# Kernel optimization log

Measured on AMD Instinct MI355X. Metric: run time of the kernel, lower is better.

## Reference

```python
import jax, jax.numpy as jnp
import numpy as np

ALPHA = 0.2  # LeakyReLU negative slope
NEG_INF = -9e15


def setup_inputs() -> dict:
    key = jax.random.key(0)
    k1, k2, k3, k4 = jax.random.split(key, 4)
    B, N, F_IN, F_OUT = 2, 4096, 128, 64
    h = jax.random.normal(k1, (B, N, F_IN), dtype=jnp.float32)
    adj = jax.random.randint(k2, (N, N), 0, 2, dtype=jnp.int32)
    W = jax.random.normal(k3, (F_IN, F_OUT), dtype=jnp.float32) * (1.414 / np.sqrt(F_IN))
    a = jax.random.normal(k4, (2 * F_OUT, 1), dtype=jnp.float32) * 0.1
    return {"h": h, "adj": adj, "W": W, "a": a}


def reference(h, adj, W, a):
    # h: (B, N, F_in), adj: (N, N), W: (F_in, F_out), a: (2*F_out, 1)
    Wh = jnp.einsum("bnf,fo->bno", h, W)  # (B, N, F_out)
    F_out = W.shape[1]
    a1 = a[:F_out, 0]   # attends to source node i
    a2 = a[F_out:, 0]   # attends to target node j
    # e_ij = leakyrelu(a1.Wh_i + a2.Wh_j)  -- rank-1 decomposition of the
    # original cat([Wh_i, Wh_j]) @ a, identical math without O(N^2*2F) tensor.
    s1 = Wh @ a1  # (B, N)
    s2 = Wh @ a2  # (B, N)
    e = s1[:, :, None] + s2[:, None, :]  # (B, N, N)
    e = jnp.where(e >= 0, e, ALPHA * e)  # LeakyReLU
    scores = jnp.where(adj[None, :, :] > 0, e, NEG_INF)
    attention = jax.nn.softmax(scores, axis=-1)
    # dropout=0 (eval/deterministic baseline)
    h_prime = jnp.einsum("bij,bjo->bio", attention, Wh)  # (B, N, F_out)
    return jax.nn.elu(h_prime)  # concat=True branch
```

## Files before the change

kernel.cpp:

```cpp
#include <hip/hip_runtime.h>
#include <hip/hip_bf16.h>
#include <math.h>

#define NB 2
#define NN 4096
#define FIN 128
#define FOUT 64
#define LALPHA 0.2f

#define WS_S1   0
#define WS_S2   (NB*NN)
#define WS_WHT  (2*NB*NN)

typedef __attribute__((ext_vector_type(8))) short short8;
typedef __attribute__((ext_vector_type(4))) float f32x4;

static __device__ inline unsigned int pack2bf(float x, float y) {
    float2 f2; f2.x = x; f2.y = y;
    __hip_bfloat162 pp = __float22bfloat162_rn(f2);
    return *reinterpret_cast<unsigned int*>(&pp);
}

__global__ __launch_bounds__(256) void k1_proj(const float* __restrict__ h,
                                               const float* __restrict__ W,
                                               const float* __restrict__ a,
                                               float* __restrict__ ws) {
    __shared__ float tbuf[4][68];
    int gid  = blockIdx.x * 256 + threadIdx.x;
    int wid  = gid >> 6;
    int lane = threadIdx.x & 63;
    int w    = threadIdx.x >> 6;
    const float* hrow = h + (size_t)wid * FIN;
    float h0 = hrow[lane];
    float h1 = hrow[64 + lane];
    float acc = 0.f;
#pragma unroll
    for (int f = 0; f < 64; ++f) {
        float hf = __shfl(h0, f);
        acc = fmaf(hf, W[f * FOUT + lane], acc);
    }
#pragma unroll
    for (int f = 0; f < 64; ++f) {
        float hf = __shfl(h1, f);
        acc = fmaf(hf, W[(64 + f) * FOUT + lane], acc);
    }
    tbuf[w][lane] = acc;
    float v1 = acc * a[lane];
    float v2 = acc * a[FOUT + lane];
#pragma unroll
    for (int off = 32; off; off >>= 1) {
        v1 += __shfl_xor(v1, off);
        v2 += __shfl_xor(v2, off);
    }
    if (lane == 0) {
        ws[WS_S1 + wid] = v1;
        ws[WS_S2 + wid] = v2;
    }
    __syncthreads();
    if (threadIdx.x < 64) {
        int f = threadIdx.x;
        int wid0 = blockIdx.x * 4;
        int b  = wid0 >> 12;
        int n0 = wid0 & (NN - 1);
        unsigned short* whT = (unsigned short*)(ws + WS_WHT);
        uint2 pk;
        pk.x = pack2bf(tbuf[0][f], tbuf[1][f]);
        pk.y = pack2bf(tbuf[2][f], tbuf[3][f]);
        *(uint2*)&whT[(size_t)(b * FOUT + f) * NN + n0] = pk;
    }
}

__global__ __launch_bounds__(1024, 4) void k3_attn(const int* __restrict__ adj,
                                                   const float* __restrict__ ws,
                                                   float* __restrict__ out) {
    __shared__ float red[16][2048];
    __shared__ float lred[16][32];
    const int tid  = threadIdx.x;
    const int w    = tid >> 6;
    const int lane = tid & 63;
    const int col  = lane & 15;
    const int quad = lane >> 4;
    const int rt   = blockIdx.x;
    const int i0   = rt * 16;
    const int jbase = w * 256;

    const float* __restrict__ s1 = ws + WS_S1;
    const float* __restrict__ s2 = ws + WS_S2;
    const unsigned short* __restrict__ whT = (const unsigned short*)(ws + WS_WHT);

    float s1a[2];
#pragma unroll
    for (int b = 0; b < 2; ++b) s1a[b] = s1[b * NN + i0 + col];

    f32x4 acc[2][4];
    float lsum[2] = {0.f, 0.f};
#pragma unroll
    for (int b = 0; b < 2; ++b)
#pragma unroll
        for (int nt = 0; nt < 4; ++nt) acc[b][nt] = (f32x4)0.f;

#pragma unroll
    for (int ks = 0; ks < 8; ++ks) {
        const int j8 = jbase + ks * 32 + quad * 8;
        int4 ava = *(const int4*)&adj[(size_t)(i0 + col) * NN + j8];
        int4 avb = *(const int4*)&adj[(size_t)(i0 + col) * NN + j8 + 4];
        int am[8] = {ava.x, ava.y, ava.z, ava.w, avb.x, avb.y, avb.z, avb.w};
#pragma unroll
        for (int b = 0; b < 2; ++b) {
            float4 s2lo = *(const float4*)&s2[b * NN + j8];
            float4 s2hi = *(const float4*)&s2[b * NN + j8 + 4];
            float sj[8] = {s2lo.x, s2lo.y, s2lo.z, s2lo.w,
                           s2hi.x, s2hi.y, s2hi.z, s2hi.w};
            float p[8];
#pragma unroll
            for (int jj = 0; jj < 8; ++jj) {
                float e = s1a[b] + sj[jj];
                e = fmaxf(e, LALPHA * e);
                float pe = __expf(e);
                p[jj] = am[jj] > 0 ? pe : 0.f;
                lsum[b] += p[jj];
            }
            unsigned int pk[4];
#pragma unroll
            for (int q = 0; q < 4; ++q) pk[q] = pack2bf(p[2 * q], p[2 * q + 1]);
            short8 afrag = *(short8*)pk;
#pragma unroll
            for (int nt = 0; nt < 4; ++nt) {
                short8 bfrag = *(const short8*)
                    &whT[(size_t)(b * FOUT + nt * 16 + col) * NN + j8];
                acc[b][nt] = __builtin_amdgcn_mfma_f32_16x16x32_bf16(
                    afrag, bfrag, acc[b][nt], 0, 0, 0);
            }
        }
    }

#pragma unroll
    for (int b = 0; b < 2; ++b) {
        float v = lsum[b];
        v += __shfl_xor(v, 16);
        v += __shfl_xor(v, 32);
        if (quad == 0) lred[w][b * 16 + col] = v;
#pragma unroll
        for (int nt = 0; nt < 4; ++nt)
#pragma unroll
            for (int reg = 0; reg < 4; ++reg)
                red[w][(((b * 4 + nt) * 4 + reg) << 6) + lane] = acc[b][nt][reg];
    }
    __syncthreads();

#pragma unroll
    for (int e = 0; e < 2; ++e) {
        int flat = e * 1024 + tid;
        int f    = flat & 63;
        int r16  = (flat >> 6) & 15;
        int b    = flat >> 10;
        int q2   = r16 >> 2, reg = r16 & 3;
        int c2   = f & 15,   nt  = f >> 4;
        int ln   = q2 * 16 + c2;
        int off  = (((b * 4 + nt) * 4 + reg) << 6) + ln;
        float acv = 0.f, l = 0.f;
#pragma unroll
        for (int ww = 0; ww < 16; ++ww) {
            acv += red[ww][off];
            l   += lred[ww][b * 16 + r16];
        }
        float v = acv / l;
        out[(size_t)(((b * NN) + i0 + r16) << 6) + f] = v > 0.f ? v : (__expf(v) - 1.f);
    }
}

extern "C" void kernel_launch(void* const* d_in, const int* in_sizes, int n_in,
                              void* d_out, int out_size, void* d_ws, size_t ws_size,
                              hipStream_t stream) {
    const float* h   = (const float*)d_in[0];
    const int*   adj = (const int*)d_in[1];
    const float* W   = (const float*)d_in[2];
    const float* a   = (const float*)d_in[3];
    float* ws  = (float*)d_ws;
    float* out = (float*)d_out;

    hipLaunchKernelGGL(k1_proj, dim3(NB * NN / 4), dim3(256), 0, stream, h, W, a, ws);
    hipLaunchKernelGGL(k3_attn, dim3(256), dim3(1024), 0, stream, adj, ws, out);
}
```

Baseline: 150.4 us.

## Prepack adjacency into bitmask in projection kernel, read bits in attention

The projection kernel now also reads the int32 adjacency matrix and packs it into a 1-bit-per-edge mask in workspace, using its many small blocks. The attention kernel loads eight 32-bit words per lane instead of streaming int4 adjacency loads inside its inner loop. The aim is to move the large adjacency read out of the low-occupancy attention kernel, where it stalls the MFMA loop, into a kernel that has more parallelism. The trade-off is an extra write and read of the bitmask, plus more work and register pressure in k1. The mask test also changes from adj > 0 to adj != 0.

```diff
diff --git a/kernel.cpp b/kernel.cpp
--- a/kernel.cpp
+++ b/kernel.cpp
@@ -8,9 +8,10 @@
 #define FOUT 64
 #define LALPHA 0.2f
 
-#define WS_S1   0
-#define WS_S2   (NB*NN)
-#define WS_WHT  (2*NB*NN)
+#define WS_S1    0
+#define WS_S2    (NB*NN)
+#define WS_WHT   (2*NB*NN)
+#define WS_ABITS (WS_WHT + NB*FOUT*NN/2)
 
 typedef __attribute__((ext_vector_type(8))) short short8;
 typedef __attribute__((ext_vector_type(4))) float f32x4;
@@ -24,12 +25,21 @@
 __global__ __launch_bounds__(256) void k1_proj(const float* __restrict__ h,
                                                const float* __restrict__ W,
                                                const float* __restrict__ a,
+                                               const int* __restrict__ adj,
                                                float* __restrict__ ws) {
     __shared__ float tbuf[4][68];
     int gid  = blockIdx.x * 256 + threadIdx.x;
     int wid  = gid >> 6;
     int lane = threadIdx.x & 63;
     int w    = threadIdx.x >> 6;
+
+    int prow  = 2 * blockIdx.x + (threadIdx.x >> 7);
+    int pword = threadIdx.x & 127;
+    const int4* psrc = (const int4*)&adj[(size_t)prow * NN + pword * 32];
+    int4 pv[8];
+#pragma unroll
+    for (int k = 0; k < 8; ++k) pv[k] = psrc[k];
+
     const float* hrow = h + (size_t)wid * FIN;
     float h0 = hrow[lane];
     float h1 = hrow[64 + lane];
@@ -56,6 +66,17 @@
         ws[WS_S1 + wid] = v1;
         ws[WS_S2 + wid] = v2;
     }
+
+    unsigned int bits = 0;
+#pragma unroll
+    for (int k = 0; k < 8; ++k) {
+        bits |= (pv[k].x != 0 ? 1u : 0u) << (4 * k);
+        bits |= (pv[k].y != 0 ? 1u : 0u) << (4 * k + 1);
+        bits |= (pv[k].z != 0 ? 1u : 0u) << (4 * k + 2);
+        bits |= (pv[k].w != 0 ? 1u : 0u) << (4 * k + 3);
+    }
+    ((unsigned int*)(ws + WS_ABITS))[(size_t)prow * 128 + pword] = bits;
+
     __syncthreads();
     if (threadIdx.x < 64) {
         int f = threadIdx.x;
@@ -70,8 +91,7 @@
     }
 }
 
-__global__ __launch_bounds__(1024, 4) void k3_attn(const int* __restrict__ adj,
-                                                   const float* __restrict__ ws,
+__global__ __launch_bounds__(1024, 4) void k3_attn(const float* __restrict__ ws,
                                                    float* __restrict__ out) {
     __shared__ float red[16][2048];
     __shared__ float lred[16][32];
@@ -87,6 +107,14 @@
     const float* __restrict__ s1 = ws + WS_S1;
     const float* __restrict__ s2 = ws + WS_S2;
     const unsigned short* __restrict__ whT = (const unsigned short*)(ws + WS_WHT);
+    const unsigned int* __restrict__ abits = (const unsigned int*)(ws + WS_ABITS);
+
+    unsigned int mrow[8];
+    {
+        const int4* mp = (const int4*)&abits[(size_t)(i0 + col) * 128 + w * 8];
+        *(int4*)&mrow[0] = mp[0];
+        *(int4*)&mrow[4] = mp[1];
+    }
 
     float s1a[2];
 #pragma unroll
@@ -102,9 +130,7 @@
 #pragma unroll
     for (int ks = 0; ks < 8; ++ks) {
         const int j8 = jbase + ks * 32 + quad * 8;
-        int4 ava = *(const int4*)&adj[(size_t)(i0 + col) * NN + j8];
-        int4 avb = *(const int4*)&adj[(size_t)(i0 + col) * NN + j8 + 4];
-        int am[8] = {ava.x, ava.y, ava.z, ava.w, avb.x, avb.y, avb.z, avb.w};
+        const unsigned int mb = (mrow[ks] >> (quad * 8)) & 0xffu;
 #pragma unroll
         for (int b = 0; b < 2; ++b) {
             float4 s2lo = *(const float4*)&s2[b * NN + j8];
@@ -117,7 +143,7 @@
                 float e = s1a[b] + sj[jj];
                 e = fmaxf(e, LALPHA * e);
                 float pe = __expf(e);
-                p[jj] = am[jj] > 0 ? pe : 0.f;
+                p[jj] = ((mb >> jj) & 1u) ? pe : 0.f;
                 lsum[b] += p[jj];
             }
             unsigned int pk[4];
@@ -179,6 +205,6 @@
     float* ws  = (float*)d_ws;
     float* out = (float*)d_out;
 
-    hipLaunchKernelGGL(k1_proj, dim3(NB * NN / 4), dim3(256), 0, stream, h, W, a, ws);
-    hipLaunchKernelGGL(k3_attn, dim3(256), dim3(1024), 0, stream, adj, ws, out);
-}
+    hipLaunchKernelGGL(k1_proj, dim3(NB * NN / 4), dim3(256), 0, stream, h, W, a, adj, ws);
+    hipLaunchKernelGGL(k3_attn, dim3(256), dim3(1024), 0, stream, ws, out);
+}
```

Measured after the change: 150.0 us. Within noise of the previous version (-0.3%).
